# Kernel tuning notes

Measured on AMD Instinct MI355X. Metric: run time of the kernel, lower is better.

Reference implementation:

```python
import jax, jax.numpy as jnp
import numpy as np

N, H, P, L, E, F = 131072, 256, 32768, 16, 8, 16
FUSED = 3 * H + E + F  # 792


def setup_inputs() -> dict:
    key = jax.random.key(0)
    ks = jax.random.split(key, 8)
    return {
        "node_embs": jax.random.normal(ks[0], (N, H), jnp.float32),
        "path_nodes": jax.random.randint(ks[1], (P, L), 0, N),
        "path_lens": jax.random.randint(ks[2], (P,), 0, L + 1),
        "path_edge_feats": jax.random.normal(ks[3], (P, E), jnp.float32),
        "path_scalar_feats": jax.random.normal(ks[4], (P, F), jnp.float32),
        "W1": jax.random.normal(ks[5], (FUSED, H), jnp.float32) / np.float32(np.sqrt(FUSED)),
        "b1": jnp.zeros((H,), jnp.float32),
        "W2": jax.random.normal(ks[6], (H, 1), jnp.float32) / np.float32(np.sqrt(H)),
        "b2": jnp.zeros((1,), jnp.float32),
        "src_idx": 0,
        "dst_idx": 1,
    }


def reference(node_embs, path_nodes, path_lens, path_edge_feats, path_scalar_feats,
              W1, b1, W2, b2, src_idx, dst_idx):
    dt = node_embs.dtype
    # ragged per-path mean over node embeddings, padded to [P, L]
    mask = (jnp.arange(L)[None, :] < path_lens[:, None]).astype(dt)  # [P, L]
    gathered = node_embs[path_nodes]                                  # [P, L, H]
    denom = jnp.maximum(path_lens, 1).astype(dt)[:, None]             # [P, 1]
    path_emb = jnp.einsum('plh,pl->ph', gathered, mask) / denom       # [P, H]

    src = jnp.broadcast_to(node_embs[src_idx], (P, H))
    dst = jnp.broadcast_to(node_embs[dst_idx], (P, H))
    fused = jnp.concatenate([src, dst, path_emb, path_edge_feats, path_scalar_feats], axis=1)  # [P, FUSED]

    h = jax.nn.relu(fused @ W1 + b1)   # [P, H]
    q = (h @ W2 + b2)[:, 0]            # [P]
    # empty paths produce exactly 0.0, matching the torch branch
    return jnp.where(path_lens > 0, q, jnp.zeros((), dt))
```

## Files before the change

### kernel.cpp

```cpp
#include <hip/hip_runtime.h>

#define NN      131072
#define H       256
#define PPATHS  32768
#define LMAX    16
#define EF      8
#define FF      16
#define TP      64
#define FS      296
#define KTOT    280

__device__ __forceinline__ unsigned short f2bf(float x) {
    unsigned int u = __float_as_uint(x);
    u += 0x7fffu + ((u >> 16) & 1u);
    return (unsigned short)(u >> 16);
}

__global__ void const_kernel(const float* __restrict__ ne,
                             const float* __restrict__ W1,
                             const float* __restrict__ b1,
                             const int* __restrict__ si,
                             const int* __restrict__ di,
                             float* __restrict__ cvec) {
    __shared__ float red[256];
    const int t  = threadIdx.x;
    const int jl = t & 3, kp = t >> 2;
    const int j  = blockIdx.x * 4 + jl;
    const float* src = ne + (size_t)si[0] * H;
    const float* dst = ne + (size_t)di[0] * H;
    float c = 0.0f;
    #pragma unroll
    for (int i = 0; i < 8; ++i) {
        int k = kp + i * 64;
        float f = (k < H) ? src[k] : dst[k - H];
        c += f * W1[(size_t)k * H + j];
    }
    red[t] = c;
    __syncthreads();
    for (int s = 128; s >= 4; s >>= 1) {
        if (t < s) red[t] += red[t + s];
        __syncthreads();
    }
    if (t < 4) cvec[blockIdx.x * 4 + t] = b1[blockIdx.x * 4 + t] + red[t];
}

__global__ __launch_bounds__(256, 3) void main_kernel(
        const float* __restrict__ node_embs,
        const int*   __restrict__ path_nodes,
        const int*   __restrict__ path_lens,
        const float* __restrict__ edge_f,
        const float* __restrict__ scal_f,
        const float* __restrict__ W1,
        const float* __restrict__ W2,
        const float* __restrict__ b2,
        const float* __restrict__ cvec,
        float*       __restrict__ out) {
    __shared__ __align__(16) unsigned short feat[TP * FS];
    __shared__ int   sidx[TP * LMAX];
    __shared__ int   slen[TP];
    __shared__ float sden[TP];
    __shared__ float qpart[TP * 33];

    const int tid   = threadIdx.x;
    const int pbase = blockIdx.x * TP;

    if (tid < TP) {
        int len   = path_lens[pbase + tid];
        slen[tid] = len;
        sden[tid] = 1.0f / (float)max(len, 1);
    }
    #pragma unroll
    for (int i = 0; i < 4; ++i)
        sidx[tid + 256 * i] = path_nodes[(size_t)pbase * LMAX + tid + 256 * i];

    for (int i = tid; i < TP * 32; i += 256) {
        int p = i >> 5, s = i & 31;
        if (s < EF)
            feat[p * FS + H + s] = f2bf(edge_f[(size_t)(pbase + p) * EF + s]);
        else if (s < EF + FF)
            feat[p * FS + H + s] = f2bf(scal_f[(size_t)(pbase + p) * FF + (s - EF)]);
    }
    __syncthreads();

    const int wave = tid >> 6, lane = tid & 63;
    for (int p = wave * 16; p < wave * 16 + 16; ++p) {
        const int len = slen[p];
        const int* idx = &sidx[p * LMAX];
        float4 a0 = make_float4(0, 0, 0, 0), a1 = make_float4(0, 0, 0, 0);
        float4 a2 = make_float4(0, 0, 0, 0), a3 = make_float4(0, 0, 0, 0);
        int l = 0;
        for (; l + 3 < len; l += 4) {
            const float4 v0 = ((const float4*)(node_embs + (size_t)idx[l]     * H))[lane];
            const float4 v1 = ((const float4*)(node_embs + (size_t)idx[l + 1] * H))[lane];
            const float4 v2 = ((const float4*)(node_embs + (size_t)idx[l + 2] * H))[lane];
            const float4 v3 = ((const float4*)(node_embs + (size_t)idx[l + 3] * H))[lane];
            a0.x += v0.x; a0.y += v0.y; a0.z += v0.z; a0.w += v0.w;
            a1.x += v1.x; a1.y += v1.y; a1.z += v1.z; a1.w += v1.w;
            a2.x += v2.x; a2.y += v2.y; a2.z += v2.z; a2.w += v2.w;
            a3.x += v3.x; a3.y += v3.y; a3.z += v3.z; a3.w += v3.w;
        }
        for (; l < len; ++l) {
            const float4 v0 = ((const float4*)(node_embs + (size_t)idx[l] * H))[lane];
            a0.x += v0.x; a0.y += v0.y; a0.z += v0.z; a0.w += v0.w;
        }
        const float inv = sden[p];
        ushort4 r;
        r.x = f2bf((a0.x + a1.x + a2.x + a3.x) * inv);
        r.y = f2bf((a0.y + a1.y + a2.y + a3.y) * inv);
        r.z = f2bf((a0.z + a1.z + a2.z + a3.z) * inv);
        r.w = f2bf((a0.w + a1.w + a2.w + a3.w) * inv);
        *(ushort4*)&feat[p * FS + 4 * lane] = r;
    }
    __syncthreads();

    const int pg = tid >> 5, jg = tid & 31;
    const int p0 = pg * 8, j0 = jg * 8;

    float h[8][8];
    {
        const float4 c0 = *(const float4*)(cvec + j0);
        const float4 c1 = *(const float4*)(cvec + j0 + 4);
        #pragma unroll
        for (int pi = 0; pi < 8; ++pi) {
            h[pi][0] = c0.x; h[pi][1] = c0.y; h[pi][2] = c0.z; h[pi][3] = c0.w;
            h[pi][4] = c1.x; h[pi][5] = c1.y; h[pi][6] = c1.z; h[pi][7] = c1.w;
        }
    }

    const float* Wk = W1 + (size_t)(2 * H) * H + j0;
    for (int k = 0; k < KTOT; k += 4) {
        float w[4][8];
        #pragma unroll
        for (int ki = 0; ki < 4; ++ki) {
            const float4 wa = *(const float4*)(Wk + (size_t)(k + ki) * H);
            const float4 wb = *(const float4*)(Wk + (size_t)(k + ki) * H + 4);
            w[ki][0] = wa.x; w[ki][1] = wa.y; w[ki][2] = wa.z; w[ki][3] = wa.w;
            w[ki][4] = wb.x; w[ki][5] = wb.y; w[ki][6] = wb.z; w[ki][7] = wb.w;
        }
        #pragma unroll
        for (int pi = 0; pi < 8; ++pi) {
            const uint2 pr = *(const uint2*)&feat[(p0 + pi) * FS + k];
            float f[4];
            f[0] = __uint_as_float(pr.x << 16);
            f[1] = __uint_as_float(pr.x & 0xffff0000u);
            f[2] = __uint_as_float(pr.y << 16);
            f[3] = __uint_as_float(pr.y & 0xffff0000u);
            #pragma unroll
            for (int ki = 0; ki < 4; ++ki)
                #pragma unroll
                for (int ji = 0; ji < 8; ++ji)
                    h[pi][ji] = fmaf(f[ki], w[ki][ji], h[pi][ji]);
        }
    }

    {
        float w2v[8];
        const float4 wa = *(const float4*)(W2 + j0);
        const float4 wb = *(const float4*)(W2 + j0 + 4);
        w2v[0] = wa.x; w2v[1] = wa.y; w2v[2] = wa.z; w2v[3] = wa.w;
        w2v[4] = wb.x; w2v[5] = wb.y; w2v[6] = wb.z; w2v[7] = wb.w;
        #pragma unroll
        for (int pi = 0; pi < 8; ++pi) {
            float s = 0.0f;
            #pragma unroll
            for (int ji = 0; ji < 8; ++ji)
                s += fmaxf(h[pi][ji], 0.0f) * w2v[ji];
            qpart[(p0 + pi) * 33 + jg] = s;
        }
    }
    __syncthreads();

    if (tid < TP) {
        float s = 0.0f;
        #pragma unroll
        for (int jj = 0; jj < 32; ++jj) s += qpart[tid * 33 + jj];
        out[pbase + tid] = (slen[tid] > 0) ? (s + b2[0]) : 0.0f;
    }
}

extern "C" void kernel_launch(void* const* d_in, const int* in_sizes, int n_in,
                              void* d_out, int out_size, void* d_ws, size_t ws_size,
                              hipStream_t stream) {
    const float* node_embs  = (const float*)d_in[0];
    const int*   path_nodes = (const int*)d_in[1];
    const int*   path_lens  = (const int*)d_in[2];
    const float* edge_f     = (const float*)d_in[3];
    const float* scal_f     = (const float*)d_in[4];
    const float* W1         = (const float*)d_in[5];
    const float* b1         = (const float*)d_in[6];
    const float* W2         = (const float*)d_in[7];
    const float* b2         = (const float*)d_in[8];
    const int*   si         = (const int*)d_in[9];
    const int*   di         = (const int*)d_in[10];
    float* out  = (float*)d_out;
    float* cvec = (float*)d_ws;

    hipLaunchKernelGGL(const_kernel, dim3(64), dim3(256), 0, stream,
                       node_embs, W1, b1, si, di, cvec);
    hipLaunchKernelGGL(main_kernel, dim3(PPATHS / TP), dim3(256), 0, stream,
                       node_embs, path_nodes, path_lens, edge_f, scal_f,
                       W1, W2, b2, cvec, out);
}
```

Before: 280.1 us.

## Split into gather and bf16 MFMA GEMM kernels with pre-transposed W1

Replaces the single fused kernel with three launches. The first converts and transposes the used W1 rows to bf16, padded to K=288. The second gathers and averages node embeddings one path per wave, using shuffled indices, and writes bf16 features to a global workspace. The third runs the 280-wide projection on MFMA 16x16x32 bf16 instructions and fuses ReLU and the W2 reduction. This moves the scalar FP32 FMA GEMM onto matrix cores, at the cost of an extra global round trip for the feature matrix and two extra launches.

Result: faster. 237.1 us (-15.3%).

```diff
diff --git a/kernel.cpp b/kernel.cpp
--- a/kernel.cpp
+++ b/kernel.cpp
@@ -6,9 +6,10 @@
 #define LMAX    16
 #define EF      8
 #define FF      16
-#define TP      64
-#define FS      296
-#define KTOT    280
+#define KP      288
+
+typedef short v8s __attribute__((ext_vector_type(8)));
+typedef float v4f __attribute__((ext_vector_type(4)));
 
 __device__ __forceinline__ unsigned short f2bf(float x) {
     unsigned int u = __float_as_uint(x);
@@ -44,137 +45,139 @@
     if (t < 4) cvec[blockIdx.x * 4 + t] = b1[blockIdx.x * 4 + t] + red[t];
 }
 
-__global__ __launch_bounds__(256, 3) void main_kernel(
+__global__ void conv_kernel(const float* __restrict__ W1,
+                            unsigned short* __restrict__ W1T) {
+    const int k = blockIdx.x;
+    const int n = threadIdx.x;
+    float v = 0.0f;
+    if (k < 256)      v = W1[(size_t)(512 + k) * H + n];
+    else if (k < 280) v = W1[(size_t)(768 + (k - 256)) * H + n];
+    W1T[(size_t)n * KP + k] = f2bf(v);
+}
+
+__global__ __launch_bounds__(256) void gather_kernel(
         const float* __restrict__ node_embs,
         const int*   __restrict__ path_nodes,
         const int*   __restrict__ path_lens,
         const float* __restrict__ edge_f,
         const float* __restrict__ scal_f,
-        const float* __restrict__ W1,
+        unsigned short* __restrict__ feat) {
+    const int wave = threadIdx.x >> 6, lane = threadIdx.x & 63;
+    const int p    = blockIdx.x * 4 + wave;
+    const int len  = path_lens[p];
+    const int iv   = path_nodes[(size_t)p * LMAX + (lane & 15)];
+
+    float4 a0 = make_float4(0, 0, 0, 0), a1 = make_float4(0, 0, 0, 0);
+    float4 a2 = make_float4(0, 0, 0, 0), a3 = make_float4(0, 0, 0, 0);
+    int l = 0;
+    for (; l + 3 < len; l += 4) {
+        const int n0 = __shfl(iv, l);
+        const int n1 = __shfl(iv, l + 1);
+        const int n2 = __shfl(iv, l + 2);
+        const int n3 = __shfl(iv, l + 3);
+        const float4 v0 = ((const float4*)(node_embs + (size_t)n0 * H))[lane];
+        const float4 v1 = ((const float4*)(node_embs + (size_t)n1 * H))[lane];
+        const float4 v2 = ((const float4*)(node_embs + (size_t)n2 * H))[lane];
+        const float4 v3 = ((const float4*)(node_embs + (size_t)n3 * H))[lane];
+        a0.x += v0.x; a0.y += v0.y; a0.z += v0.z; a0.w += v0.w;
+        a1.x += v1.x; a1.y += v1.y; a1.z += v1.z; a1.w += v1.w;
+        a2.x += v2.x; a2.y += v2.y; a2.z += v2.z; a2.w += v2.w;
+        a3.x += v3.x; a3.y += v3.y; a3.z += v3.z; a3.w += v3.w;
+    }
+    for (; l < len; ++l) {
+        const int n0 = __shfl(iv, l);
+        const float4 v0 = ((const float4*)(node_embs + (size_t)n0 * H))[lane];
+        a0.x += v0.x; a0.y += v0.y; a0.z += v0.z; a0.w += v0.w;
+    }
+    const float inv = 1.0f / (float)max(len, 1);
+    ushort4 r;
+    r.x = f2bf((a0.x + a1.x + a2.x + a3.x) * inv);
+    r.y = f2bf((a0.y + a1.y + a2.y + a3.y) * inv);
+    r.z = f2bf((a0.z + a1.z + a2.z + a3.z) * inv);
+    r.w = f2bf((a0.w + a1.w + a2.w + a3.w) * inv);
+    *(ushort4*)(feat + (size_t)p * KP + 4 * lane) = r;
+
+    if (lane < 32) {
+        float v = 0.0f;
+        if (lane < EF)            v = edge_f[(size_t)p * EF + lane];
+        else if (lane < EF + FF)  v = scal_f[(size_t)p * FF + (lane - EF)];
+        feat[(size_t)p * KP + H + lane] = f2bf(v);
+    }
+}
+
+__global__ __launch_bounds__(256) void gemm_kernel(
+        const unsigned short* __restrict__ feat,
+        const unsigned short* __restrict__ W1T,
+        const float* __restrict__ cvec,
         const float* __restrict__ W2,
         const float* __restrict__ b2,
-        const float* __restrict__ cvec,
+        const int*   __restrict__ path_lens,
         float*       __restrict__ out) {
-    __shared__ __align__(16) unsigned short feat[TP * FS];
-    __shared__ int   sidx[TP * LMAX];
-    __shared__ int   slen[TP];
-    __shared__ float sden[TP];
-    __shared__ float qpart[TP * 33];
-
-    const int tid   = threadIdx.x;
-    const int pbase = blockIdx.x * TP;
-
-    if (tid < TP) {
-        int len   = path_lens[pbase + tid];
-        slen[tid] = len;
-        sden[tid] = 1.0f / (float)max(len, 1);
-    }
+    __shared__ float qpart[64][5];
+    const int wave = threadIdx.x >> 6, lane = threadIdx.x & 63;
+    const int pb   = blockIdx.x * 64;
+    const int col  = lane & 15, quad = lane >> 4;
+    const int n0   = wave * 64;
+
+    v4f acc[4][4];
+    float w2v[4];
     #pragma unroll
-    for (int i = 0; i < 4; ++i)
-        sidx[tid + 256 * i] = path_nodes[(size_t)pbase * LMAX + tid + 256 * i];
-
-    for (int i = tid; i < TP * 32; i += 256) {
-        int p = i >> 5, s = i & 31;
-        if (s < EF)
-            feat[p * FS + H + s] = f2bf(edge_f[(size_t)(pbase + p) * EF + s]);
-        else if (s < EF + FF)
-            feat[p * FS + H + s] = f2bf(scal_f[(size_t)(pbase + p) * FF + (s - EF)]);
+    for (int nt = 0; nt < 4; ++nt) {
+        const float cv = cvec[n0 + nt * 16 + col];
+        w2v[nt] = W2[n0 + nt * 16 + col];
+        #pragma unroll
+        for (int mt = 0; mt < 4; ++mt)
+            acc[mt][nt] = (v4f){cv, cv, cv, cv};
+    }
+
+    const unsigned short* Abase = feat + (size_t)(pb + col) * KP + quad * 8;
+    const unsigned short* Bbase = W1T + (size_t)(n0 + col) * KP + quad * 8;
+
+    for (int k0 = 0; k0 < KP; k0 += 32) {
+        v8s a[4], b[4];
+        #pragma unroll
+        for (int mt = 0; mt < 4; ++mt)
+            a[mt] = *(const v8s*)(Abase + (size_t)(mt * 16) * KP + k0);
+        #pragma unroll
+        for (int nt = 0; nt < 4; ++nt)
+            b[nt] = *(const v8s*)(Bbase + (size_t)(nt * 16) * KP + k0);
+        #pragma unroll
+        for (int mt = 0; mt < 4; ++mt)
+            #pragma unroll
+            for (int nt = 0; nt < 4; ++nt)
+                acc[mt][nt] = __builtin_amdgcn_mfma_f32_16x16x32_bf16(
+                                  a[mt], b[nt], acc[mt][nt], 0, 0, 0);
+    }
+
+    #pragma unroll
+    for (int mt = 0; mt < 4; ++mt) {
+        float s[4];
+        #pragma unroll
+        for (int r = 0; r < 4; ++r) {
+            float v = 0.0f;
+            #pragma unroll
+            for (int nt = 0; nt < 4; ++nt)
+                v += fmaxf(acc[mt][nt][r], 0.0f) * w2v[nt];
+            s[r] = v;
+        }
+        #pragma unroll
+        for (int off = 1; off < 16; off <<= 1) {
+            #pragma unroll
+            for (int r = 0; r < 4; ++r)
+                s[r] += __shfl_xor(s[r], off);
+        }
+        if (col == 0) {
+            #pragma unroll
+            for (int r = 0; r < 4; ++r)
+                qpart[mt * 16 + quad * 4 + r][wave] = s[r];
+        }
     }
     __syncthreads();
 
-    const int wave = tid >> 6, lane = tid & 63;
-    for (int p = wave * 16; p < wave * 16 + 16; ++p) {
-        const int len = slen[p];
-        const int* idx = &sidx[p * LMAX];
-        float4 a0 = make_float4(0, 0, 0, 0), a1 = make_float4(0, 0, 0, 0);
-        float4 a2 = make_float4(0, 0, 0, 0), a3 = make_float4(0, 0, 0, 0);
-        int l = 0;
-        for (; l + 3 < len; l += 4) {
-            const float4 v0 = ((const float4*)(node_embs + (size_t)idx[l]     * H))[lane];
-            const float4 v1 = ((const float4*)(node_embs + (size_t)idx[l + 1] * H))[lane];
-            const float4 v2 = ((const float4*)(node_embs + (size_t)idx[l + 2] * H))[lane];
-            const float4 v3 = ((const float4*)(node_embs + (size_t)idx[l + 3] * H))[lane];
-            a0.x += v0.x; a0.y += v0.y; a0.z += v0.z; a0.w += v0.w;
-            a1.x += v1.x; a1.y += v1.y; a1.z += v1.z; a1.w += v1.w;
-            a2.x += v2.x; a2.y += v2.y; a2.z += v2.z; a2.w += v2.w;
-            a3.x += v3.x; a3.y += v3.y; a3.z += v3.z; a3.w += v3.w;
-        }
-        for (; l < len; ++l) {
-            const float4 v0 = ((const float4*)(node_embs + (size_t)idx[l] * H))[lane];
-            a0.x += v0.x; a0.y += v0.y; a0.z += v0.z; a0.w += v0.w;
-        }
-        const float inv = sden[p];
-        ushort4 r;
-        r.x = f2bf((a0.x + a1.x + a2.x + a3.x) * inv);
-        r.y = f2bf((a0.y + a1.y + a2.y + a3.y) * inv);
-        r.z = f2bf((a0.z + a1.z + a2.z + a3.z) * inv);
-        r.w = f2bf((a0.w + a1.w + a2.w + a3.w) * inv);
-        *(ushort4*)&feat[p * FS + 4 * lane] = r;
-    }
-    __syncthreads();
-
-    const int pg = tid >> 5, jg = tid & 31;
-    const int p0 = pg * 8, j0 = jg * 8;
-
-    float h[8][8];
-    {
-        const float4 c0 = *(const float4*)(cvec + j0);
-        const float4 c1 = *(const float4*)(cvec + j0 + 4);
-        #pragma unroll
-        for (int pi = 0; pi < 8; ++pi) {
-            h[pi][0] = c0.x; h[pi][1] = c0.y; h[pi][2] = c0.z; h[pi][3] = c0.w;
-            h[pi][4] = c1.x; h[pi][5] = c1.y; h[pi][6] = c1.z; h[pi][7] = c1.w;
-        }
-    }
-
-    const float* Wk = W1 + (size_t)(2 * H) * H + j0;
-    for (int k = 0; k < KTOT; k += 4) {
-        float w[4][8];
-        #pragma unroll
-        for (int ki = 0; ki < 4; ++ki) {
-            const float4 wa = *(const float4*)(Wk + (size_t)(k + ki) * H);
-            const float4 wb = *(const float4*)(Wk + (size_t)(k + ki) * H + 4);
-            w[ki][0] = wa.x; w[ki][1] = wa.y; w[ki][2] = wa.z; w[ki][3] = wa.w;
-            w[ki][4] = wb.x; w[ki][5] = wb.y; w[ki][6] = wb.z; w[ki][7] = wb.w;
-        }
-        #pragma unroll
-        for (int pi = 0; pi < 8; ++pi) {
-            const uint2 pr = *(const uint2*)&feat[(p0 + pi) * FS + k];
-            float f[4];
-            f[0] = __uint_as_float(pr.x << 16);
-            f[1] = __uint_as_float(pr.x & 0xffff0000u);
-            f[2] = __uint_as_float(pr.y << 16);
-            f[3] = __uint_as_float(pr.y & 0xffff0000u);
-            #pragma unroll
-            for (int ki = 0; ki < 4; ++ki)
-                #pragma unroll
-                for (int ji = 0; ji < 8; ++ji)
-                    h[pi][ji] = fmaf(f[ki], w[ki][ji], h[pi][ji]);
-        }
-    }
-
-    {
-        float w2v[8];
-        const float4 wa = *(const float4*)(W2 + j0);
-        const float4 wb = *(const float4*)(W2 + j0 + 4);
-        w2v[0] = wa.x; w2v[1] = wa.y; w2v[2] = wa.z; w2v[3] = wa.w;
-        w2v[4] = wb.x; w2v[5] = wb.y; w2v[6] = wb.z; w2v[7] = wb.w;
-        #pragma unroll
-        for (int pi = 0; pi < 8; ++pi) {
-            float s = 0.0f;
-            #pragma unroll
-            for (int ji = 0; ji < 8; ++ji)
-                s += fmaxf(h[pi][ji], 0.0f) * w2v[ji];
-            qpart[(p0 + pi) * 33 + jg] = s;
-        }
-    }
-    __syncthreads();
-
-    if (tid < TP) {
-        float s = 0.0f;
-        #pragma unroll
-        for (int jj = 0; jj < 32; ++jj) s += qpart[tid * 33 + jj];
-        out[pbase + tid] = (slen[tid] > 0) ? (s + b2[0]) : 0.0f;
+    if (threadIdx.x < 64) {
+        const int t = threadIdx.x;
+        const float q = qpart[t][0] + qpart[t][1] + qpart[t][2] + qpart[t][3] + b2[0];
+        out[pb + t] = (path_lens[pb + t] > 0) ? q : 0.0f;
     }
 }
 
@@ -192,12 +195,17 @@
     const float* b2         = (const float*)d_in[8];
     const int*   si         = (const int*)d_in[9];
     const int*   di         = (const int*)d_in[10];
-    float* out  = (float*)d_out;
-    float* cvec = (float*)d_ws;
+    float* out = (float*)d_out;
+
+    float*          cvec = (float*)d_ws;
+    unsigned short* W1T  = (unsigned short*)((char*)d_ws + 1024);
+    unsigned short* feat = (unsigned short*)((char*)d_ws + 148480);
 
     hipLaunchKernelGGL(const_kernel, dim3(64), dim3(256), 0, stream,
                        node_embs, W1, b1, si, di, cvec);
-    hipLaunchKernelGGL(main_kernel, dim3(PPATHS / TP), dim3(256), 0, stream,
-                       node_embs, path_nodes, path_lens, edge_f, scal_f,
-                       W1, W2, b2, cvec, out);
-}
+    hipLaunchKernelGGL(conv_kernel, dim3(KP), dim3(256), 0, stream, W1, W1T);
+    hipLaunchKernelGGL(gather_kernel, dim3(PPATHS / 4), dim3(256), 0, stream,
+                       node_embs, path_nodes, path_lens, edge_f, scal_f, feat);
+    hipLaunchKernelGGL(gemm_kernel, dim3(PPATHS / 64), dim3(256), 0, stream,
+                       feat, W1T, cvec, W2, b2, path_lens, out);
+}
```
